# Optimization experiments

Measured on AMD Instinct MI355X. Metric: run time of the kernel, lower is better.

## Reference

```python
import jax, jax.numpy as jnp
import numpy as np

EPS_STOP = 1e-4  # convergence tolerance from the torch module


def setup_inputs() -> dict:
    key = jax.random.key(0)
    k1, k2, k3 = jax.random.split(key, 3)
    m, n, B = 70, 100, 4096
    # Build A and derive S, W exactly as ISTA.weights_init does, so the
    # iteration matrix is a contraction (spectral radius < 1).
    A = jax.random.normal(k1, (m, n), dtype=jnp.float32) / np.sqrt(m)
    alpha = (jnp.linalg.norm(A, 2) ** 2) * 1.001
    S = jnp.eye(n, dtype=jnp.float32) - (1.0 / alpha) * (A.T @ A)   # [n, n]
    W = (1.0 / alpha) * A.T                                          # [n, m]
    thr = (jnp.ones((1, 1), dtype=jnp.float32) * 0.05 / alpha)       # learned threshold
    y = jax.random.normal(k2, (B, m), dtype=jnp.float32)
    return {"y": y, "S": S, "W": W, "thr": thr, "numIter": 1000}


def soft_thr(x, theta):
    # F.relu(x - theta) - F.relu(-x - theta)
    return jax.nn.relu(x - theta) - jax.nn.relu(-x - theta)


def reference(y, S, W, thr, numIter):
    B = y.shape[0]
    n = S.shape[0]
    # torch.mm(W, y.T).T == y @ W.T ; constant across iterations
    Wy = y @ W.T                                   # [B, n]
    d0 = jnp.zeros((B, n), dtype=y.dtype)
    big = jnp.array(jnp.inf, dtype=y.dtype)

    def cond_fn(carry):
        i, d, diff = carry
        return jnp.logical_and(i < numIter, diff >= EPS_STOP)

    def body_fn(carry):
        i, d, _ = carry
        # torch.mm(S, d.T).T == d @ S.T
        d_new = soft_thr(d @ S.T + Wy, thr)
        diff = jnp.linalg.norm(d_new - d)
        return (i + 1, d_new, diff)

    _, d, _ = jax.lax.while_loop(cond_fn, body_fn, (0, d0, big))
    return d
```

## Files before the change

kernel.cpp:

```cpp
#include <hip/hip_runtime.h>
#include <hip/hip_bf16.h>


#define ROWS     16
#define KPAD     128
#define N_DIM    100
#define M_DIM    70
#define NTHREADS 256

typedef __attribute__((ext_vector_type(8))) short short8;
typedef __attribute__((ext_vector_type(4))) float f32x4;

static __device__ __forceinline__ unsigned short f2bf(float f) {
    unsigned u = __float_as_uint(f);
    u += 0x7FFF + ((u >> 16) & 1);
    return (unsigned short)(u >> 16);
}
static __device__ __forceinline__ float bf2f(unsigned short b) {
    return __uint_as_float(((unsigned)b) << 16);
}
static __device__ __forceinline__ unsigned cvt_pk_bf16(float a, float b) {
    unsigned r;
    asm("v_cvt_pk_bf16_f32 %0, %1, %2" : "=v"(r) : "v"(a), "v"(b));
    return r;
}
static __device__ __forceinline__ float med3f(float x, float lo, float hi) {
    float r;
    asm("v_med3_f32 %0, %1, %2, %3" : "=v"(r) : "v"(x), "v"(lo), "v"(hi));
    return r;
}

__global__ __launch_bounds__(NTHREADS)
void ista_mfma5(const float* __restrict__ y,
                const float* __restrict__ S,
                const float* __restrict__ W,
                const float* __restrict__ thr,
                const int*   __restrict__ numIter,
                float* __restrict__ out)
{
    __shared__ __align__(16) unsigned short dh[2][ROWS * KPAD];
    __shared__ __align__(16) unsigned short dl[2][ROWS * KPAD];

    const int t    = threadIdx.x;
    const int wv   = t >> 6;
    const int l    = t & 63;
    const int l15  = l & 15;
    const int lg   = l >> 4;
    const int row0 = blockIdx.x * ROWS;
    const float th  = thr[0];
    const float nth = -th;
    const int iters = numIter[0];
    const unsigned swz = (unsigned)((l15 & 7) << 4);

    short8 Sh[2][4], Sl[2][4];
    #pragma unroll
    for (int n2 = 0; n2 < 2; ++n2) {
        const int jg = (wv * 2 + n2) * 16 + l15;
        #pragma unroll
        for (int kt = 0; kt < 4; ++kt) {
            #pragma unroll
            for (int i = 0; i < 8; ++i) {
                const int k = kt * 32 + lg * 8 + i;
                const float v = (jg < N_DIM && k < N_DIM) ? S[jg * N_DIM + k] : 0.f;
                const unsigned short hb = f2bf(v);
                Sh[n2][kt][i] = (short)hb;
                Sl[n2][kt][i] = (short)f2bf(v - bf2f(hb));
            }
        }
    }

    f32x4 Wyr[2];
    #pragma unroll
    for (int n2 = 0; n2 < 2; ++n2) {
        #pragma unroll
        for (int q = 0; q < 4; ++q) {
            const int j = wv * 32 + n2 * 16 + lg * 4 + q;
            float acc = 0.f;
            if (j < N_DIM) {
                const float* yr = y + (size_t)(row0 + l15) * M_DIM;
                const float* wr = W + (size_t)j * M_DIM;
                #pragma unroll 10
                for (int m = 0; m < M_DIM; ++m) acc = fmaf(yr[m], wr[m], acc);
            }
            Wyr[n2][q] = acc;
        }
    }

    for (int idx = t; idx < ROWS * KPAD; idx += NTHREADS) {
        dh[0][idx] = 0; dl[0][idx] = 0;
    }
    __syncthreads();

    unsigned roff[4];
    #pragma unroll
    for (int kt = 0; kt < 4; ++kt)
        roff[kt] = ((unsigned)(l15 * 256 + kt * 64 + lg * 16)) ^ swz;
    unsigned woff[2];
    #pragma unroll
    for (int n2 = 0; n2 < 2; ++n2)
        woff[n2] = ((unsigned)(l15 * 256 + wv * 64 + n2 * 32 + lg * 8)) ^ swz;

    int cur = 0;
    for (int it = 0; it < iters; ++it) {
        const char* rh = (const char*)dh[cur];
        const char* rl = (const char*)dl[cur];
        char* wh = (char*)dh[cur ^ 1];
        char* wl = (char*)dl[cur ^ 1];

        short8 Bh[4], Bl[4];
        #pragma unroll
        for (int kt = 0; kt < 4; ++kt) {
            Bh[kt] = *(const short8*)(rh + roff[kt]);
            Bl[kt] = *(const short8*)(rl + roff[kt]);
        }

        f32x4 Chh[2] = { Wyr[0], Wyr[1] };
        f32x4 Chl[2] = { {0,0,0,0}, {0,0,0,0} };
        f32x4 Clh[2] = { {0,0,0,0}, {0,0,0,0} };
        #pragma unroll
        for (int kt = 0; kt < 4; ++kt) {
            #pragma unroll
            for (int n2 = 0; n2 < 2; ++n2)
                Chh[n2] = __builtin_amdgcn_mfma_f32_16x16x32_bf16(Sh[n2][kt], Bh[kt], Chh[n2], 0, 0, 0);
            #pragma unroll
            for (int n2 = 0; n2 < 2; ++n2)
                Chl[n2] = __builtin_amdgcn_mfma_f32_16x16x32_bf16(Sh[n2][kt], Bl[kt], Chl[n2], 0, 0, 0);
            #pragma unroll
            for (int n2 = 0; n2 < 2; ++n2)
                Clh[n2] = __builtin_amdgcn_mfma_f32_16x16x32_bf16(Sl[n2][kt], Bh[kt], Clh[n2], 0, 0, 0);
        }

        #pragma unroll
        for (int n2 = 0; n2 < 2; ++n2) {
            float r0, r1, r2, r3;
            {
                const float s0 = Chh[n2][0] + Chl[n2][0] + Clh[n2][0];
                const float s1 = Chh[n2][1] + Chl[n2][1] + Clh[n2][1];
                const float s2 = Chh[n2][2] + Chl[n2][2] + Clh[n2][2];
                const float s3 = Chh[n2][3] + Chl[n2][3] + Clh[n2][3];
                r0 = s0 - med3f(s0, nth, th);
                r1 = s1 - med3f(s1, nth, th);
                r2 = s2 - med3f(s2, nth, th);
                r3 = s3 - med3f(s3, nth, th);
            }
            const unsigned h01 = cvt_pk_bf16(r0, r1);
            const unsigned h23 = cvt_pk_bf16(r2, r3);
            const float l0 = r0 - __uint_as_float(h01 << 16);
            const float l1 = r1 - __uint_as_float(h01 & 0xFFFF0000u);
            const float l2 = r2 - __uint_as_float(h23 << 16);
            const float l3 = r3 - __uint_as_float(h23 & 0xFFFF0000u);
            const unsigned lo01 = cvt_pk_bf16(l0, l1);
            const unsigned lo23 = cvt_pk_bf16(l2, l3);
            *(uint2*)(wh + woff[n2]) = make_uint2(h01, h23);
            *(uint2*)(wl + woff[n2]) = make_uint2(lo01, lo23);
        }

        __syncthreads();
        cur ^= 1;
    }

    for (int idx = t; idx < ROWS * N_DIM; idx += NTHREADS) {
        const int r = idx / N_DIM;
        const int j = idx - r * N_DIM;
        const unsigned off = ((unsigned)(r * 256 + j * 2)) ^ ((unsigned)((r & 7) << 4));
        const float v = bf2f(*(const unsigned short*)((const char*)dh[cur] + off))
                      + bf2f(*(const unsigned short*)((const char*)dl[cur] + off));
        out[(size_t)(row0 + r) * N_DIM + j] = v;
    }
}

extern "C" void kernel_launch(void* const* d_in, const int* in_sizes, int n_in,
                              void* d_out, int out_size, void* d_ws, size_t ws_size,
                              hipStream_t stream) {
    const float* y       = (const float*)d_in[0];
    const float* S       = (const float*)d_in[1];
    const float* W       = (const float*)d_in[2];
    const float* thr     = (const float*)d_in[3];
    const int*   numIter = (const int*)d_in[4];
    float* out = (float*)d_out;

    const int Brows = in_sizes[0] / M_DIM;
    const int nblk  = Brows / ROWS;
    ista_mfma5<<<nblk, NTHREADS, 0, stream>>>(y, S, W, thr, numIter, out);
}
```

Measured before the change: 530.4 us.

## Split K dimension across two wave groups with LDS partial-sum exchange

Doubles the block to 512 threads (8 waves). Each group of four waves computes half the K tiles of the S·d product, and the two halves exchange partial sums through a new shared buffer before the soft-threshold. This halves the serial MFMA chain per wave on the iteration-critical path and raises wave count per CU. In exchange it adds a second __syncthreads per iteration plus LDS round-trip traffic, which lengthens the per-iteration latency chain.

```diff
diff --git a/kernel.cpp b/kernel.cpp
--- a/kernel.cpp
+++ b/kernel.cpp
@@ -6,7 +6,7 @@
 #define KPAD     128
 #define N_DIM    100
 #define M_DIM    70
-#define NTHREADS 256
+#define NTHREADS 512
 
 typedef __attribute__((ext_vector_type(8))) short short8;
 typedef __attribute__((ext_vector_type(4))) float f32x4;
@@ -30,8 +30,8 @@
     return r;
 }
 
-__global__ __launch_bounds__(NTHREADS)
-void ista_mfma5(const float* __restrict__ y,
+__global__ __launch_bounds__(NTHREADS, 2)
+void ista_mfma6(const float* __restrict__ y,
                 const float* __restrict__ S,
                 const float* __restrict__ W,
                 const float* __restrict__ thr,
@@ -40,49 +40,56 @@
 {
     __shared__ __align__(16) unsigned short dh[2][ROWS * KPAD];
     __shared__ __align__(16) unsigned short dl[2][ROWS * KPAD];
+    __shared__ __align__(16) float psum[8][64 * 4];
 
     const int t    = threadIdx.x;
     const int wv   = t >> 6;
     const int l    = t & 63;
     const int l15  = l & 15;
     const int lg   = l >> 4;
+    const int g    = wv & 3;
+    const int up   = wv >> 2;
+    const int ktb  = up * 2;
     const int row0 = blockIdx.x * ROWS;
     const float th  = thr[0];
     const float nth = -th;
     const int iters = numIter[0];
     const unsigned swz = (unsigned)((l15 & 7) << 4);
 
-    short8 Sh[2][4], Sl[2][4];
+    short8 Sh[2][2], Sl[2][2];
     #pragma unroll
     for (int n2 = 0; n2 < 2; ++n2) {
-        const int jg = (wv * 2 + n2) * 16 + l15;
+        const int jg = g * 32 + n2 * 16 + l15;
         #pragma unroll
-        for (int kt = 0; kt < 4; ++kt) {
+        for (int kc = 0; kc < 2; ++kc) {
+            const int kt = ktb + kc;
             #pragma unroll
             for (int i = 0; i < 8; ++i) {
                 const int k = kt * 32 + lg * 8 + i;
                 const float v = (jg < N_DIM && k < N_DIM) ? S[jg * N_DIM + k] : 0.f;
                 const unsigned short hb = f2bf(v);
-                Sh[n2][kt][i] = (short)hb;
-                Sl[n2][kt][i] = (short)f2bf(v - bf2f(hb));
+                Sh[n2][kc][i] = (short)hb;
+                Sl[n2][kc][i] = (short)f2bf(v - bf2f(hb));
             }
         }
     }
 
-    f32x4 Wyr[2];
-    #pragma unroll
-    for (int n2 = 0; n2 < 2; ++n2) {
+    f32x4 Wyr[2] = { {0,0,0,0}, {0,0,0,0} };
+    if (!up) {
         #pragma unroll
-        for (int q = 0; q < 4; ++q) {
-            const int j = wv * 32 + n2 * 16 + lg * 4 + q;
-            float acc = 0.f;
-            if (j < N_DIM) {
-                const float* yr = y + (size_t)(row0 + l15) * M_DIM;
-                const float* wr = W + (size_t)j * M_DIM;
-                #pragma unroll 10
-                for (int m = 0; m < M_DIM; ++m) acc = fmaf(yr[m], wr[m], acc);
+        for (int n2 = 0; n2 < 2; ++n2) {
+            #pragma unroll
+            for (int q = 0; q < 4; ++q) {
+                const int j = g * 32 + n2 * 16 + lg * 4 + q;
+                float acc = 0.f;
+                if (j < N_DIM) {
+                    const float* yr = y + (size_t)(row0 + l15) * M_DIM;
+                    const float* wr = W + (size_t)j * M_DIM;
+                    #pragma unroll 10
+                    for (int m = 0; m < M_DIM; ++m) acc = fmaf(yr[m], wr[m], acc);
+                }
+                Wyr[n2][q] = acc;
             }
-            Wyr[n2][q] = acc;
         }
     }
 
@@ -91,14 +98,13 @@
     }
     __syncthreads();
 
-    unsigned roff[4];
+    unsigned roff[2];
     #pragma unroll
-    for (int kt = 0; kt < 4; ++kt)
-        roff[kt] = ((unsigned)(l15 * 256 + kt * 64 + lg * 16)) ^ swz;
-    unsigned woff[2];
-    #pragma unroll
-    for (int n2 = 0; n2 < 2; ++n2)
-        woff[n2] = ((unsigned)(l15 * 256 + wv * 64 + n2 * 32 + lg * 8)) ^ swz;
+    for (int kc = 0; kc < 2; ++kc)
+        roff[kc] = ((unsigned)(l15 * 256 + (ktb + kc) * 64 + lg * 16)) ^ swz;
+    const unsigned woff = ((unsigned)(l15 * 256 + g * 64 + up * 32 + lg * 8)) ^ swz;
+    float* pme = &psum[wv][l * 4];
+    const float* ppa = &psum[wv ^ 4][l * 4];
 
     int cur = 0;
     for (int it = 0; it < iters; ++it) {
@@ -107,53 +113,61 @@
         char* wh = (char*)dh[cur ^ 1];
         char* wl = (char*)dl[cur ^ 1];
 
-        short8 Bh[4], Bl[4];
+        short8 Bh[2], Bl[2];
         #pragma unroll
-        for (int kt = 0; kt < 4; ++kt) {
-            Bh[kt] = *(const short8*)(rh + roff[kt]);
-            Bl[kt] = *(const short8*)(rl + roff[kt]);
+        for (int kc = 0; kc < 2; ++kc) {
+            Bh[kc] = *(const short8*)(rh + roff[kc]);
+            Bl[kc] = *(const short8*)(rl + roff[kc]);
         }
 
         f32x4 Chh[2] = { Wyr[0], Wyr[1] };
         f32x4 Chl[2] = { {0,0,0,0}, {0,0,0,0} };
         f32x4 Clh[2] = { {0,0,0,0}, {0,0,0,0} };
         #pragma unroll
-        for (int kt = 0; kt < 4; ++kt) {
+        for (int kc = 0; kc < 2; ++kc) {
             #pragma unroll
             for (int n2 = 0; n2 < 2; ++n2)
-                Chh[n2] = __builtin_amdgcn_mfma_f32_16x16x32_bf16(Sh[n2][kt], Bh[kt], Chh[n2], 0, 0, 0);
+                Chh[n2] = __builtin_amdgcn_mfma_f32_16x16x32_bf16(Sh[n2][kc], Bh[kc], Chh[n2], 0, 0, 0);
             #pragma unroll
             for (int n2 = 0; n2 < 2; ++n2)
-                Chl[n2] = __builtin_amdgcn_mfma_f32_16x16x32_bf16(Sh[n2][kt], Bl[kt], Chl[n2], 0, 0, 0);
+                Chl[n2] = __builtin_amdgcn_mfma_f32_16x16x32_bf16(Sh[n2][kc], Bl[kc], Chl[n2], 0, 0, 0);
             #pragma unroll
             for (int n2 = 0; n2 < 2; ++n2)
-                Clh[n2] = __builtin_amdgcn_mfma_f32_16x16x32_bf16(Sl[n2][kt], Bh[kt], Clh[n2], 0, 0, 0);
+                Clh[n2] = __builtin_amdgcn_mfma_f32_16x16x32_bf16(Sl[n2][kc], Bh[kc], Clh[n2], 0, 0, 0);
         }
 
+        f32x4 P0, P1;
         #pragma unroll
-        for (int n2 = 0; n2 < 2; ++n2) {
-            float r0, r1, r2, r3;
-            {
-                const float s0 = Chh[n2][0] + Chl[n2][0] + Clh[n2][0];
-                const float s1 = Chh[n2][1] + Chl[n2][1] + Clh[n2][1];
-                const float s2 = Chh[n2][2] + Chl[n2][2] + Clh[n2][2];
-                const float s3 = Chh[n2][3] + Chl[n2][3] + Clh[n2][3];
-                r0 = s0 - med3f(s0, nth, th);
-                r1 = s1 - med3f(s1, nth, th);
-                r2 = s2 - med3f(s2, nth, th);
-                r3 = s3 - med3f(s3, nth, th);
-            }
-            const unsigned h01 = cvt_pk_bf16(r0, r1);
-            const unsigned h23 = cvt_pk_bf16(r2, r3);
-            const float l0 = r0 - __uint_as_float(h01 << 16);
-            const float l1 = r1 - __uint_as_float(h01 & 0xFFFF0000u);
-            const float l2 = r2 - __uint_as_float(h23 << 16);
-            const float l3 = r3 - __uint_as_float(h23 & 0xFFFF0000u);
-            const unsigned lo01 = cvt_pk_bf16(l0, l1);
-            const unsigned lo23 = cvt_pk_bf16(l2, l3);
-            *(uint2*)(wh + woff[n2]) = make_uint2(h01, h23);
-            *(uint2*)(wl + woff[n2]) = make_uint2(lo01, lo23);
+        for (int q = 0; q < 4; ++q) {
+            P0[q] = Chh[0][q] + Chl[0][q] + Clh[0][q];
+            P1[q] = Chh[1][q] + Chl[1][q] + Clh[1][q];
         }
+        *(f32x4*)pme = up ? P0 : P1;
+        __syncthreads();
+
+        const f32x4 mine  = up ? P1 : P0;
+        const f32x4 other = *(const f32x4*)ppa;
+        float r0, r1, r2, r3;
+        {
+            const float s0 = mine[0] + other[0];
+            const float s1 = mine[1] + other[1];
+            const float s2 = mine[2] + other[2];
+            const float s3 = mine[3] + other[3];
+            r0 = s0 - med3f(s0, nth, th);
+            r1 = s1 - med3f(s1, nth, th);
+            r2 = s2 - med3f(s2, nth, th);
+            r3 = s3 - med3f(s3, nth, th);
+        }
+        const unsigned h01 = cvt_pk_bf16(r0, r1);
+        const unsigned h23 = cvt_pk_bf16(r2, r3);
+        const float l0 = r0 - __uint_as_float(h01 << 16);
+        const float l1 = r1 - __uint_as_float(h01 & 0xFFFF0000u);
+        const float l2 = r2 - __uint_as_float(h23 << 16);
+        const float l3 = r3 - __uint_as_float(h23 & 0xFFFF0000u);
+        const unsigned lo01 = cvt_pk_bf16(l0, l1);
+        const unsigned lo23 = cvt_pk_bf16(l2, l3);
+        *(uint2*)(wh + woff) = make_uint2(h01, h23);
+        *(uint2*)(wl + woff) = make_uint2(lo01, lo23);
 
         __syncthreads();
         cur ^= 1;
@@ -181,5 +195,5 @@
 
     const int Brows = in_sizes[0] / M_DIM;
     const int nblk  = Brows / ROWS;
-    ista_mfma5<<<nblk, NTHREADS, 0, stream>>>(y, S, W, thr, numIter, out);
+    ista_mfma6<<<nblk, NTHREADS, 0, stream>>>(y, S, W, thr, numIter, out);
 }
```

After: 620.5 us. 1.17x slower.

## Split output columns across eight waves, one 16-column tile per wave

Applied to the files above, without the earlier changes.

Doubles the block to 512 threads (8 waves) so each wave owns a single 16-column output tile instead of two, halving per-wave MFMA chain length and S register footprint per iteration. This shortens the serial critical path of each ISTA iteration, since per-block latency dominates with only 256 blocks. The cost is more waves per barrier and more redundant LDS reads of the B operand across waves.

```diff
diff --git a/kernel.cpp b/kernel.cpp
--- a/kernel.cpp
+++ b/kernel.cpp
@@ -6,7 +6,7 @@
 #define KPAD     128
 #define N_DIM    100
 #define M_DIM    70
-#define NTHREADS 256
+#define NTHREADS 512
 
 typedef __attribute__((ext_vector_type(8))) short short8;
 typedef __attribute__((ext_vector_type(4))) float f32x4;
@@ -30,8 +30,8 @@
     return r;
 }
 
-__global__ __launch_bounds__(NTHREADS)
-void ista_mfma5(const float* __restrict__ y,
+__global__ __launch_bounds__(NTHREADS, 2)
+void ista_mfma8(const float* __restrict__ y,
                 const float* __restrict__ S,
                 const float* __restrict__ W,
                 const float* __restrict__ thr,
@@ -52,10 +52,9 @@
     const int iters = numIter[0];
     const unsigned swz = (unsigned)((l15 & 7) << 4);
 
-    short8 Sh[2][4], Sl[2][4];
-    #pragma unroll
-    for (int n2 = 0; n2 < 2; ++n2) {
-        const int jg = (wv * 2 + n2) * 16 + l15;
+    short8 Sh[4], Sl[4];
+    {
+        const int jg = wv * 16 + l15;
         #pragma unroll
         for (int kt = 0; kt < 4; ++kt) {
             #pragma unroll
@@ -63,27 +62,24 @@
                 const int k = kt * 32 + lg * 8 + i;
                 const float v = (jg < N_DIM && k < N_DIM) ? S[jg * N_DIM + k] : 0.f;
                 const unsigned short hb = f2bf(v);
-                Sh[n2][kt][i] = (short)hb;
-                Sl[n2][kt][i] = (short)f2bf(v - bf2f(hb));
+                Sh[kt][i] = (short)hb;
+                Sl[kt][i] = (short)f2bf(v - bf2f(hb));
             }
         }
     }
 
-    f32x4 Wyr[2];
+    f32x4 Wyr;
     #pragma unroll
-    for (int n2 = 0; n2 < 2; ++n2) {
-        #pragma unroll
-        for (int q = 0; q < 4; ++q) {
-            const int j = wv * 32 + n2 * 16 + lg * 4 + q;
-            float acc = 0.f;
-            if (j < N_DIM) {
-                const float* yr = y + (size_t)(row0 + l15) * M_DIM;
-                const float* wr = W + (size_t)j * M_DIM;
-                #pragma unroll 10
-                for (int m = 0; m < M_DIM; ++m) acc = fmaf(yr[m], wr[m], acc);
-            }
-            Wyr[n2][q] = acc;
+    for (int q = 0; q < 4; ++q) {
+        const int j = wv * 16 + lg * 4 + q;
+        float acc = 0.f;
+        if (j < N_DIM) {
+            const float* yr = y + (size_t)(row0 + l15) * M_DIM;
+            const float* wr = W + (size_t)j * M_DIM;
+            #pragma unroll 10
+            for (int m = 0; m < M_DIM; ++m) acc = fmaf(yr[m], wr[m], acc);
         }
+        Wyr[q] = acc;
     }
 
     for (int idx = t; idx < ROWS * KPAD; idx += NTHREADS) {
@@ -95,10 +91,7 @@
     #pragma unroll
     for (int kt = 0; kt < 4; ++kt)
         roff[kt] = ((unsigned)(l15 * 256 + kt * 64 + lg * 16)) ^ swz;
-    unsigned woff[2];
-    #pragma unroll
-    for (int n2 = 0; n2 < 2; ++n2)
-        woff[n2] = ((unsigned)(l15 * 256 + wv * 64 + n2 * 32 + lg * 8)) ^ swz;
+    const unsigned woff = ((unsigned)(l15 * 256 + wv * 32 + lg * 8)) ^ swz;
 
     int cur = 0;
     for (int it = 0; it < iters; ++it) {
@@ -114,46 +107,37 @@
             Bl[kt] = *(const short8*)(rl + roff[kt]);
         }
 
-        f32x4 Chh[2] = { Wyr[0], Wyr[1] };
-        f32x4 Chl[2] = { {0,0,0,0}, {0,0,0,0} };
-        f32x4 Clh[2] = { {0,0,0,0}, {0,0,0,0} };
+        f32x4 Chh = Wyr;
+        f32x4 Chl = {0,0,0,0};
+        f32x4 Clh = {0,0,0,0};
         #pragma unroll
         for (int kt = 0; kt < 4; ++kt) {
-            #pragma unroll
-            for (int n2 = 0; n2 < 2; ++n2)
-                Chh[n2] = __builtin_amdgcn_mfma_f32_16x16x32_bf16(Sh[n2][kt], Bh[kt], Chh[n2], 0, 0, 0);
-            #pragma unroll
-            for (int n2 = 0; n2 < 2; ++n2)
-                Chl[n2] = __builtin_amdgcn_mfma_f32_16x16x32_bf16(Sh[n2][kt], Bl[kt], Chl[n2], 0, 0, 0);
-            #pragma unroll
-            for (int n2 = 0; n2 < 2; ++n2)
-                Clh[n2] = __builtin_amdgcn_mfma_f32_16x16x32_bf16(Sl[n2][kt], Bh[kt], Clh[n2], 0, 0, 0);
+            Chh = __builtin_amdgcn_mfma_f32_16x16x32_bf16(Sh[kt], Bh[kt], Chh, 0, 0, 0);
+            Chl = __builtin_amdgcn_mfma_f32_16x16x32_bf16(Sh[kt], Bl[kt], Chl, 0, 0, 0);
+            Clh = __builtin_amdgcn_mfma_f32_16x16x32_bf16(Sl[kt], Bh[kt], Clh, 0, 0, 0);
         }
 
-        #pragma unroll
-        for (int n2 = 0; n2 < 2; ++n2) {
-            float r0, r1, r2, r3;
-            {
-                const float s0 = Chh[n2][0] + Chl[n2][0] + Clh[n2][0];
-                const float s1 = Chh[n2][1] + Chl[n2][1] + Clh[n2][1];
-                const float s2 = Chh[n2][2] + Chl[n2][2] + Clh[n2][2];
-                const float s3 = Chh[n2][3] + Chl[n2][3] + Clh[n2][3];
-                r0 = s0 - med3f(s0, nth, th);
-                r1 = s1 - med3f(s1, nth, th);
-                r2 = s2 - med3f(s2, nth, th);
-                r3 = s3 - med3f(s3, nth, th);
-            }
-            const unsigned h01 = cvt_pk_bf16(r0, r1);
-            const unsigned h23 = cvt_pk_bf16(r2, r3);
-            const float l0 = r0 - __uint_as_float(h01 << 16);
-            const float l1 = r1 - __uint_as_float(h01 & 0xFFFF0000u);
-            const float l2 = r2 - __uint_as_float(h23 << 16);
-            const float l3 = r3 - __uint_as_float(h23 & 0xFFFF0000u);
-            const unsigned lo01 = cvt_pk_bf16(l0, l1);
-            const unsigned lo23 = cvt_pk_bf16(l2, l3);
-            *(uint2*)(wh + woff[n2]) = make_uint2(h01, h23);
-            *(uint2*)(wl + woff[n2]) = make_uint2(lo01, lo23);
+        float r0, r1, r2, r3;
+        {
+            const float s0 = Chh[0] + Chl[0] + Clh[0];
+            const float s1 = Chh[1] + Chl[1] + Clh[1];
+            const float s2 = Chh[2] + Chl[2] + Clh[2];
+            const float s3 = Chh[3] + Chl[3] + Clh[3];
+            r0 = s0 - med3f(s0, nth, th);
+            r1 = s1 - med3f(s1, nth, th);
+            r2 = s2 - med3f(s2, nth, th);
+            r3 = s3 - med3f(s3, nth, th);
         }
+        const unsigned h01 = cvt_pk_bf16(r0, r1);
+        const unsigned h23 = cvt_pk_bf16(r2, r3);
+        const float l0 = r0 - __uint_as_float(h01 << 16);
+        const float l1 = r1 - __uint_as_float(h01 & 0xFFFF0000u);
+        const float l2 = r2 - __uint_as_float(h23 << 16);
+        const float l3 = r3 - __uint_as_float(h23 & 0xFFFF0000u);
+        const unsigned lo01 = cvt_pk_bf16(l0, l1);
+        const unsigned lo23 = cvt_pk_bf16(l2, l3);
+        *(uint2*)(wh + woff) = make_uint2(h01, h23);
+        *(uint2*)(wl + woff) = make_uint2(lo01, lo23);
 
         __syncthreads();
         cur ^= 1;
@@ -181,5 +165,5 @@
 
     const int Brows = in_sizes[0] / M_DIM;
     const int nblk  = Brows / ROWS;
-    ista_mfma5<<<nblk, NTHREADS, 0, stream>>>(y, S, W, thr, numIter, out);
+    ista_mfma8<<<nblk, NTHREADS, 0, stream>>>(y, S, W, thr, numIter, out);
 }
```

Measured after the change: 464.4 us. 12.4% less time.
